# Kernel optimization log

Hardware: AMD Instinct MI355X
Metric: run time of the kernel (lower is better)

## Reference

```python
import jax, jax.numpy as jnp
import numpy as np

B, N, D = 4, 2048, 1024  # in_features == out_features required by the original code path
SPARSITY = 0.01


def setup_inputs() -> dict:
    key = jax.random.key(0)
    k1, k2, k3 = jax.random.split(key, 3)
    x = jax.random.normal(k1, (B, N, D), dtype=jnp.float32)
    # Reproduce FrequencyLinearLayer.__init__: sparse top-k frequency weights.
    spatial = jax.random.normal(k2, (D, D), dtype=jnp.float32) * 0.02
    freq = jnp.fft.fft(spatial, axis=-1)  # complex64, (out, in) consumed as (D_in, D_out)
    k = int(D * SPARSITY)
    mag = jnp.abs(freq)
    kth = jax.lax.top_k(mag, k)[0][:, -1:]  # k-th largest magnitude per row
    w_sparse = jnp.where(mag >= kth, freq, 0.0 + 0.0j)
    bias = jax.random.normal(k3, (D,), dtype=jnp.float32) * 0.01
    return {
        "x": x,
        "w_freq_real": jnp.real(w_sparse).astype(jnp.float32),
        "w_freq_imag": jnp.imag(w_sparse).astype(jnp.float32),
        "bias": bias,
    }


def reference(x, w_freq_real, w_freq_imag, bias):
    # y = real(IFFT(FFT(x) @ W_freq)) + bias
    # The original materializes a (B,N,D_in,D_out) complex intermediate via
    # unsqueeze*multiply -> sum; that is exactly a complex matmul, expressed here as einsum.
    w = jax.lax.complex(w_freq_real, w_freq_imag)            # (D_in, D_out) complex64
    x_freq = jnp.fft.fft(x, axis=-1)                          # (B, N, D_in) complex64
    y_freq = jnp.einsum('bnd,do->bno', x_freq, w)             # (B, N, D_out)
    y = jnp.real(jnp.fft.ifft(y_freq, axis=-1))               # (B, N, D_out) float32
    return y + bias
```

## Files before the change

kernel.cpp:

```cpp
#include <hip/hip_runtime.h>
#include <hip/hip_bf16.h>
#include <math.h>

#define DD 1024
#define BT 8192
#define TWO_PI 6.28318530717958647692f

typedef float f32x4 __attribute__((ext_vector_type(4)));
typedef short bf16x8 __attribute__((ext_vector_type(8)));
typedef unsigned short u16x8 __attribute__((ext_vector_type(8)));
typedef unsigned short u16x4 __attribute__((ext_vector_type(4)));
typedef const __attribute__((address_space(1))) void g_void;
typedef __attribute__((address_space(3))) void l_void;

__device__ __forceinline__ unsigned short f2bf(float f) {
  unsigned int u = __float_as_uint(f);
  unsigned int r = (u + 0x7FFFu + ((u >> 16) & 1u)) >> 16;
  return (unsigned short)r;
}

__global__ __launch_bounds__(256) void transpose_W_kernel(
    const float* __restrict__ Wr, const float* __restrict__ Wi,
    float2* __restrict__ Wt) {
  __shared__ float tr[64][65];
  __shared__ float ti[64][65];
  const int k0 = blockIdx.y * 64, o0 = blockIdx.x * 64;
  for (int q = threadIdx.x; q < 64 * 64; q += 256) {
    int r = q >> 6, c = q & 63;
    tr[r][c] = Wr[(size_t)(k0 + r) * DD + o0 + c];
    ti[r][c] = Wi[(size_t)(k0 + r) * DD + o0 + c];
  }
  __syncthreads();
  for (int q = threadIdx.x; q < 64 * 64; q += 256) {
    int r = q >> 6, c = q & 63;
    Wt[(size_t)(o0 + r) * DD + k0 + c] = make_float2(tr[c][r], ti[c][r]);
  }
}

__global__ __launch_bounds__(256) void build_T_kernel(
    const float2* __restrict__ Wt, float2* __restrict__ T) {
  __shared__ float2 tw[DD];
  __shared__ int    kidx[64];
  __shared__ float2 wval[64];
  __shared__ int    sc[256];
  const int o = blockIdx.x, tid = threadIdx.x;

  for (int j = tid; j < DD; j += 256) {
    float s, c;
    sincosf((TWO_PI / DD) * (float)j, &s, &c);
    tw[j] = make_float2(c, s);
  }
  int cnt = 0;
  float2 wl[4];
  int    kl[4];
#pragma unroll
  for (int q = 0; q < 4; q++) {
    int k = tid + q * 256;
    float2 w = Wt[(size_t)o * DD + k];
    if (w.x != 0.f || w.y != 0.f) { wl[cnt] = w; kl[cnt] = k; cnt++; }
  }
  sc[tid] = cnt;
  __syncthreads();
#pragma unroll
  for (int dstep = 1; dstep < 256; dstep <<= 1) {
    int v = (tid >= dstep) ? sc[tid - dstep] : 0;
    __syncthreads();
    sc[tid] += v;
    __syncthreads();
  }
  int p = sc[tid] - cnt;
  for (int q = 0; q < cnt; q++) { kidx[p + q] = kl[q]; wval[p + q] = wl[q]; }
  __syncthreads();
  const int nnz = sc[255];
  for (int d = tid; d < DD; d += 256) {
    float re = 0.f, im = 0.f;
    for (int j = 0; j < nnz; j++) {
      int    k  = kidx[j];
      float2 w  = wval[j];
      float2 cs = tw[(k * d) & (DD - 1)];
      re += w.x * cs.x + w.y * cs.y;
      im += w.y * cs.x - w.x * cs.y;
    }
    T[(size_t)o * DD + d] = make_float2(re, im);
  }
}

__global__ __launch_bounds__(256) void transpose_T_kernel(
    const float2* __restrict__ T, unsigned short* __restrict__ TT) {
  __shared__ float2 tile[64][65];
  const int o0 = blockIdx.x * 64, d0 = blockIdx.y * 64;
  for (int q = threadIdx.x; q < 64 * 64; q += 256) {
    int r = q >> 6, c = q & 63;
    tile[r][c] = T[(size_t)(o0 + r) * DD + d0 + c];
  }
  __syncthreads();
  for (int q = threadIdx.x; q < 64 * 64; q += 256) {
    int r = q >> 6, c = q & 63;
    float2 v = tile[c][r];
    TT[(size_t)(d0 + r) * 2048 + o0 + c]        = f2bf(v.x);
    TT[(size_t)(d0 + r) * 2048 + 1024 + o0 + c] = f2bf(v.y);
  }
}

__global__ __launch_bounds__(256) void gen_CS_kernel(unsigned short* __restrict__ CS) {
  int idx = blockIdx.x * 256 + threadIdx.x;
  int m = idx >> 10, o = idx & 1023;
  float s, c;
  sincosf((TWO_PI / DD) * (float)((m * o) & (DD - 1)), &s, &c);
  CS[(size_t)m * 2048 + o]        = f2bf(c);
  CS[(size_t)m * 2048 + 1024 + o] = f2bf(-s);
}

__global__ __launch_bounds__(256) void convert_x_kernel(
    const float* __restrict__ X, unsigned short* __restrict__ Xb) {
  size_t i = (size_t)blockIdx.x * 256 + threadIdx.x;
  const float4* p = (const float4*)(X + i * 8);
  float4 a = p[0], b = p[1];
  u16x8 v;
  v[0] = f2bf(a.x); v[1] = f2bf(a.y); v[2] = f2bf(a.z); v[3] = f2bf(a.w);
  v[4] = f2bf(b.x); v[5] = f2bf(b.y); v[6] = f2bf(b.z); v[7] = f2bf(b.w);
  *(u16x8*)(Xb + i * 8) = v;
}

template <int LDK, int MODE, int GX>
__global__ __launch_bounds__(256) void mfma_nt_kernel(
    const unsigned short* __restrict__ A,
    const unsigned short* __restrict__ B,
    const float* __restrict__ bias,
    float* __restrict__ Out, float scale, int ldo, int kLen) {
  __shared__ __align__(16) unsigned short Asm[2][128 * 32];
  __shared__ __align__(16) unsigned short Bsm[2][128 * 32];
  const int tid  = threadIdx.x;
  const int wave = tid >> 6, lane = tid & 63;
  const int wr = wave >> 1, wc = wave & 1;

  const int L     = blockIdx.x;
  const int chunk = gridDim.x >> 3;
  const int W     = (L & 7) * chunk + (L >> 3);
  const int tx    = W % GX;
  const int tyz   = W / GX;
  const int ty    = (MODE == 2) ? (tyz & 7) : tyz;
  const int tz    = (MODE == 2) ? (tyz >> 3) : 0;

  const int row0 = ty * 128;
  const int col0 = tx * 128;
  const int kBeg = tz * kLen;

  f32x4 acc[4][4] = {};

  for (int k0 = kBeg; k0 < kBeg + kLen; k0 += 64) {
    __syncthreads();
#pragma unroll
    for (int h = 0; h < 2; h++) {
#pragma unroll
      for (int is = 0; is < 2; is++) {
        int e = is * 256 + tid;
        int r = e >> 2, c = (e & 3) * 8;
        const unsigned short* ga = A + (size_t)(row0 + r) * LDK + k0 + h * 32 + c;
        const unsigned short* gb = B + (size_t)(col0 + r) * LDK + k0 + h * 32 + c;
        __builtin_amdgcn_global_load_lds((g_void*)ga, (l_void*)(Asm[h] + is * 2048 + wave * 512), 16, 0, 0);
        __builtin_amdgcn_global_load_lds((g_void*)gb, (l_void*)(Bsm[h] + is * 2048 + wave * 512), 16, 0, 0);
      }
    }
    __syncthreads();

#pragma unroll
    for (int h = 0; h < 2; h++) {
      bf16x8 af[4], bfr[4];
#pragma unroll
      for (int i = 0; i < 4; i++) {
        int ra = wr * 64 + i * 16 + (lane & 15);
        af[i]  = *(const bf16x8*)&Asm[h][ra * 32 + (lane >> 4) * 8];
        int rb = wc * 64 + i * 16 + (lane & 15);
        bfr[i] = *(const bf16x8*)&Bsm[h][rb * 32 + (lane >> 4) * 8];
      }
#pragma unroll
      for (int i = 0; i < 4; i++)
#pragma unroll
        for (int j = 0; j < 4; j++)
          acc[i][j] = __builtin_amdgcn_mfma_f32_16x16x32_bf16(af[i], bfr[j], acc[i][j], 0, 0, 0);
    }
  }

  const int crow0 = row0 + wr * 64;
  const int ccol0 = col0 + wc * 64;
  if (MODE == 2) {
    float* O = Out + (size_t)tz * DD * DD;
#pragma unroll
    for (int i = 0; i < 4; i++)
#pragma unroll
      for (int j = 0; j < 4; j++) {
        int cc = ccol0 + j * 16 + (lane & 15);
#pragma unroll
        for (int v = 0; v < 4; v++) {
          int rr = crow0 + i * 16 + (lane >> 4) * 4 + v;
          O[(size_t)rr * ldo + cc] = acc[i][j][v];
        }
      }
  } else {
    float bv[4];
#pragma unroll
    for (int j = 0; j < 4; j++)
      bv[j] = bias[ccol0 + j * 16 + (lane & 15)];
#pragma unroll
    for (int i = 0; i < 4; i++)
#pragma unroll
      for (int j = 0; j < 4; j++) {
        int cc = ccol0 + j * 16 + (lane & 15);
#pragma unroll
        for (int v = 0; v < 4; v++) {
          int rr = crow0 + i * 16 + (lane >> 4) * 4 + v;
          Out[(size_t)rr * ldo + cc] = acc[i][j][v] * scale + bv[j];
        }
      }
  }
}

__global__ __launch_bounds__(256) void reduce_M_kernel(
    const float* __restrict__ P, unsigned short* __restrict__ Mb) {
  const size_t NE = (size_t)DD * DD;
  size_t i = ((size_t)blockIdx.x * 256 + threadIdx.x) * 4;
  float4 s = *(const float4*)(P + i);
#pragma unroll
  for (int z = 1; z < 4; z++) {
    float4 p = *(const float4*)(P + z * NE + i);
    s.x += p.x; s.y += p.y; s.z += p.z; s.w += p.w;
  }
  const float inv = 1.0f / (float)DD;
  u16x4 v;
  v[0] = f2bf(s.x * inv); v[1] = f2bf(s.y * inv);
  v[2] = f2bf(s.z * inv); v[3] = f2bf(s.w * inv);
  *(u16x4*)(Mb + i) = v;
}

extern "C" void kernel_launch(void* const* d_in, const int* in_sizes, int n_in,
                              void* d_out, int out_size, void* d_ws, size_t ws_size,
                              hipStream_t stream) {
  const float* x    = (const float*)d_in[0];
  const float* wrp  = (const float*)d_in[1];
  const float* wip  = (const float*)d_in[2];
  const float* bias = (const float*)d_in[3];
  float*       y    = (float*)d_out;

  char* ws = (char*)d_ws;
  const size_t MB = 1024 * 1024;
  float2*         Wt = (float2*)(ws + 0);
  float2*         T  = (float2*)(ws + 8  * MB);
  unsigned short* TT = (unsigned short*)(ws + 16 * MB);
  unsigned short* CS = (unsigned short*)(ws + 20 * MB);
  unsigned short* Mb = (unsigned short*)(ws + 24 * MB);
  float*          P  = (float*)(ws + 0);
  unsigned short* Xb = (unsigned short*)(ws + 0);

  transpose_W_kernel<<<dim3(16, 16), 256, 0, stream>>>(wrp, wip, Wt);
  build_T_kernel<<<DD, 256, 0, stream>>>(Wt, T);
  transpose_T_kernel<<<dim3(16, 16), 256, 0, stream>>>(T, TT);
  gen_CS_kernel<<<4096, 256, 0, stream>>>(CS);
  mfma_nt_kernel<2048, 2, 8><<<256, 256, 0, stream>>>(
      CS, TT, nullptr, P, 1.0f, DD, 512);
  reduce_M_kernel<<<DD * DD / (256 * 4), 256, 0, stream>>>(P, Mb);
  convert_x_kernel<<<4096, 256, 0, stream>>>(x, Xb);
  mfma_nt_kernel<1024, 0, 8><<<512, 256, 0, stream>>>(
      Xb, Mb, bias, y, 1.0f, DD, 1024);
}
```

Baseline: 106.6 us.

## Parameterize GEMM tile width, shrink K step, drop XCD-swizzled block mapping

```diff
diff --git a/kernel.cpp b/kernel.cpp
--- a/kernel.cpp
+++ b/kernel.cpp
@@ -122,74 +122,69 @@
   *(u16x8*)(Xb + i * 8) = v;
 }
 
-template <int LDK, int MODE, int GX>
+template <int LDK, int MODE, int BN>
 __global__ __launch_bounds__(256) void mfma_nt_kernel(
     const unsigned short* __restrict__ A,
     const unsigned short* __restrict__ B,
     const float* __restrict__ bias,
     float* __restrict__ Out, float scale, int ldo, int kLen) {
-  __shared__ __align__(16) unsigned short Asm[2][128 * 32];
-  __shared__ __align__(16) unsigned short Bsm[2][128 * 32];
+  constexpr int NJ = BN / 32;
+  __shared__ __align__(16) unsigned short Asm[128 * 32];
+  __shared__ __align__(16) unsigned short Bsm[BN * 32];
   const int tid  = threadIdx.x;
   const int wave = tid >> 6, lane = tid & 63;
   const int wr = wave >> 1, wc = wave & 1;
-
-  const int L     = blockIdx.x;
-  const int chunk = gridDim.x >> 3;
-  const int W     = (L & 7) * chunk + (L >> 3);
-  const int tx    = W % GX;
-  const int tyz   = W / GX;
-  const int ty    = (MODE == 2) ? (tyz & 7) : tyz;
-  const int tz    = (MODE == 2) ? (tyz >> 3) : 0;
-
-  const int row0 = ty * 128;
-  const int col0 = tx * 128;
-  const int kBeg = tz * kLen;
-
-  f32x4 acc[4][4] = {};
-
-  for (int k0 = kBeg; k0 < kBeg + kLen; k0 += 64) {
-    __syncthreads();
-#pragma unroll
-    for (int h = 0; h < 2; h++) {
-#pragma unroll
-      for (int is = 0; is < 2; is++) {
-        int e = is * 256 + tid;
-        int r = e >> 2, c = (e & 3) * 8;
-        const unsigned short* ga = A + (size_t)(row0 + r) * LDK + k0 + h * 32 + c;
-        const unsigned short* gb = B + (size_t)(col0 + r) * LDK + k0 + h * 32 + c;
-        __builtin_amdgcn_global_load_lds((g_void*)ga, (l_void*)(Asm[h] + is * 2048 + wave * 512), 16, 0, 0);
-        __builtin_amdgcn_global_load_lds((g_void*)gb, (l_void*)(Bsm[h] + is * 2048 + wave * 512), 16, 0, 0);
-      }
-    }
-    __syncthreads();
-
-#pragma unroll
-    for (int h = 0; h < 2; h++) {
-      bf16x8 af[4], bfr[4];
-#pragma unroll
-      for (int i = 0; i < 4; i++) {
-        int ra = wr * 64 + i * 16 + (lane & 15);
-        af[i]  = *(const bf16x8*)&Asm[h][ra * 32 + (lane >> 4) * 8];
-        int rb = wc * 64 + i * 16 + (lane & 15);
-        bfr[i] = *(const bf16x8*)&Bsm[h][rb * 32 + (lane >> 4) * 8];
-      }
-#pragma unroll
-      for (int i = 0; i < 4; i++)
-#pragma unroll
-        for (int j = 0; j < 4; j++)
-          acc[i][j] = __builtin_amdgcn_mfma_f32_16x16x32_bf16(af[i], bfr[j], acc[i][j], 0, 0, 0);
-    }
+  const int row0 = blockIdx.y * 128;
+  const int col0 = blockIdx.x * BN;
+  const int kBeg = (MODE == 2) ? blockIdx.z * kLen : 0;
+  const int kEnd = (MODE == 2) ? kBeg + kLen : LDK;
+
+  f32x4 acc[4][NJ] = {};
+
+  for (int k0 = kBeg; k0 < kEnd; k0 += 32) {
+    __syncthreads();
+#pragma unroll
+    for (int is = 0; is < 2; is++) {
+      int e = is * 256 + tid;
+      int r = e >> 2, c = (e & 3) * 8;
+      const unsigned short* ga = A + (size_t)(row0 + r) * LDK + k0 + c;
+      __builtin_amdgcn_global_load_lds((g_void*)ga, (l_void*)(Asm + is * 2048 + wave * 512), 16, 0, 0);
+    }
+#pragma unroll
+    for (int is = 0; is < BN / 64; is++) {
+      int e = is * 256 + tid;
+      int r = e >> 2, c = (e & 3) * 8;
+      const unsigned short* gb = B + (size_t)(col0 + r) * LDK + k0 + c;
+      __builtin_amdgcn_global_load_lds((g_void*)gb, (l_void*)(Bsm + is * 2048 + wave * 512), 16, 0, 0);
+    }
+    __syncthreads();
+
+    bf16x8 af[4], bfr[NJ];
+#pragma unroll
+    for (int i = 0; i < 4; i++) {
+      int ra = wr * 64 + i * 16 + (lane & 15);
+      af[i]  = *(const bf16x8*)&Asm[ra * 32 + (lane >> 4) * 8];
+    }
+#pragma unroll
+    for (int j = 0; j < NJ; j++) {
+      int rb = wc * (BN / 2) + j * 16 + (lane & 15);
+      bfr[j] = *(const bf16x8*)&Bsm[rb * 32 + (lane >> 4) * 8];
+    }
+#pragma unroll
+    for (int i = 0; i < 4; i++)
+#pragma unroll
+      for (int j = 0; j < NJ; j++)
+        acc[i][j] = __builtin_amdgcn_mfma_f32_16x16x32_bf16(af[i], bfr[j], acc[i][j], 0, 0, 0);
   }
 
   const int crow0 = row0 + wr * 64;
-  const int ccol0 = col0 + wc * 64;
+  const int ccol0 = col0 + wc * (BN / 2);
   if (MODE == 2) {
-    float* O = Out + (size_t)tz * DD * DD;
+    float* O = Out + (size_t)blockIdx.z * DD * DD;
 #pragma unroll
     for (int i = 0; i < 4; i++)
 #pragma unroll
-      for (int j = 0; j < 4; j++) {
+      for (int j = 0; j < NJ; j++) {
         int cc = ccol0 + j * 16 + (lane & 15);
 #pragma unroll
         for (int v = 0; v < 4; v++) {
@@ -198,14 +193,14 @@
         }
       }
   } else {
-    float bv[4];
-#pragma unroll
-    for (int j = 0; j < 4; j++)
+    float bv[NJ];
+#pragma unroll
+    for (int j = 0; j < NJ; j++)
       bv[j] = bias[ccol0 + j * 16 + (lane & 15)];
 #pragma unroll
     for (int i = 0; i < 4; i++)
 #pragma unroll
-      for (int j = 0; j < 4; j++) {
+      for (int j = 0; j < NJ; j++) {
         int cc = ccol0 + j * 16 + (lane & 15);
 #pragma unroll
         for (int v = 0; v < 4; v++) {
@@ -256,10 +251,10 @@
   build_T_kernel<<<DD, 256, 0, stream>>>(Wt, T);
   transpose_T_kernel<<<dim3(16, 16), 256, 0, stream>>>(T, TT);
   gen_CS_kernel<<<4096, 256, 0, stream>>>(CS);
-  mfma_nt_kernel<2048, 2, 8><<<256, 256, 0, stream>>>(
+  mfma_nt_kernel<2048, 2, 128><<<dim3(8, 8, 4), 256, 0, stream>>>(
       CS, TT, nullptr, P, 1.0f, DD, 512);
   reduce_M_kernel<<<DD * DD / (256 * 4), 256, 0, stream>>>(P, Mb);
   convert_x_kernel<<<4096, 256, 0, stream>>>(x, Xb);
-  mfma_nt_kernel<1024, 0, 8><<<512, 256, 0, stream>>>(
+  mfma_nt_kernel<1024, 0, 64><<<dim3(16, 64), 256, 0, stream>>>(
       Xb, Mb, bias, y, 1.0f, DD, 1024);
 }
```

Result: no change. 108.4 us (+1.7%).
